# Optimization experiments

Hardware: AMD Instinct MI355X
Metric: run time of the kernel (lower is better)

The kernel has to match this reference:

```python
import jax, jax.numpy as jnp
import numpy as np

B, S, H = 2, 2048, 4096
NH, NKV, HD = 32, 8, 128
Q_SIZE, KV_SIZE = NH * HD, NKV * HD
ROPE_THETA = 10000.0


def setup_inputs() -> dict:
    key = jax.random.key(0)
    k1, k2, k3 = jax.random.split(key, 3)
    positions = jnp.tile(jnp.arange(S, dtype=jnp.int64 if jax.config.jax_enable_x64 else jnp.int32), (B, 1))
    hidden_states = jax.random.normal(k1, (B, S, H), dtype=jnp.float32)
    w_qkv = jax.random.normal(k2, (H, Q_SIZE + 2 * KV_SIZE), dtype=jnp.float32) * 0.02
    w_o = jax.random.normal(k3, (Q_SIZE, H), dtype=jnp.float32) * 0.02
    return {"positions": positions, "hidden_states": hidden_states, "w_qkv": w_qkv, "w_o": w_o}


def _apply_rope(x, positions):
    # x: [B, S, nheads, HD]; neox-style rotate-half RoPE
    half = HD // 2
    inv_freq = 1.0 / (ROPE_THETA ** (jnp.arange(0, half, dtype=jnp.float32) / half))
    freqs = positions.astype(jnp.float32)[..., None] * inv_freq  # [B, S, HD/2]
    cos = jnp.cos(freqs)[:, :, None, :]  # [B, S, 1, HD/2]
    sin = jnp.sin(freqs)[:, :, None, :]
    x1, x2 = x[..., :half], x[..., half:]
    return jnp.concatenate([x1 * cos - x2 * sin, x2 * cos + x1 * sin], axis=-1)


def reference(positions, hidden_states, w_qkv, w_o):
    qkv = jnp.einsum("bsh,hd->bsd", hidden_states, w_qkv)
    q = qkv[..., :Q_SIZE].reshape(B, S, NH, HD)
    k = qkv[..., Q_SIZE:Q_SIZE + KV_SIZE].reshape(B, S, NKV, HD)
    v = qkv[..., Q_SIZE + KV_SIZE:].reshape(B, S, NKV, HD)

    q = _apply_rope(q, positions)
    k = _apply_rope(k, positions)

    # GQA: expand kv heads to match query heads
    rep = NH // NKV
    k = jnp.repeat(k, rep, axis=2)  # [B, S, NH, HD]
    v = jnp.repeat(v, rep, axis=2)

    scale = 1.0 / jnp.sqrt(jnp.float32(HD))
    scores = jnp.einsum("bqhd,bkhd->bhqk", q, k) * scale  # [B, NH, S, S]
    causal = jnp.tril(jnp.ones((S, S), dtype=bool))
    scores = jnp.where(causal[None, None], scores, jnp.finfo(scores.dtype).min)
    probs = jax.nn.softmax(scores, axis=-1)

    attn = jnp.einsum("bhqk,bkhd->bqhd", probs, v).reshape(B, S, Q_SIZE)
    return jnp.einsum("bsd,dh->bsh", attn, w_o)
```

## Files before the change

### kernel.cpp

```cpp
#include <hip/hip_runtime.h>
#include <hip/hip_bf16.h>
#include <math.h>


typedef __attribute__((ext_vector_type(8))) __bf16 bf16x8;
typedef __attribute__((ext_vector_type(4))) float floatx4;

__device__ __forceinline__ floatx4 mfma16(bf16x8 a, bf16x8 b, floatx4 c) {
    return __builtin_amdgcn_mfma_f32_16x16x32_bf16(a, b, c, 0, 0, 0);
}

__device__ __forceinline__ void load_lds16(const __hip_bfloat16* g,
                                           __hip_bfloat16* lds_base_uniform) {
    __builtin_amdgcn_global_load_lds(
        (const __attribute__((address_space(1))) unsigned int*)g,
        (__attribute__((address_space(3))) unsigned int*)lds_base_uniform,
        16, 0, 0);
}

__global__ __launch_bounds__(256)
void convert_kernel(const float* __restrict__ in, __hip_bfloat16* __restrict__ out,
                    int n) {
    int i = (blockIdx.x * 256 + threadIdx.x) * 4;
    if (i >= n) return;
    float4 v = *(const float4*)(in + i);
    union { __hip_bfloat16 h[4]; uint2 u; } pk;
    pk.h[0] = __float2bfloat16(v.x);
    pk.h[1] = __float2bfloat16(v.y);
    pk.h[2] = __float2bfloat16(v.z);
    pk.h[3] = __float2bfloat16(v.w);
    *(uint2*)(out + i) = pk.u;
}

__global__ __launch_bounds__(256)
void transpose_f32_bf16_kernel(const float* __restrict__ in,
                               __hip_bfloat16* __restrict__ out, int R, int C) {
    __shared__ __hip_bfloat16 tile[64][65];
    const int r0 = blockIdx.y * 64, c0 = blockIdx.x * 64;
    const int t = threadIdx.x;
    #pragma unroll
    for (int i = 0; i < 16; ++i) {
        int idx = t + 256 * i;
        int rl = idx >> 6, cl = idx & 63;
        tile[rl][cl] = __float2bfloat16(in[(size_t)(r0 + rl) * C + (c0 + cl)]);
    }
    __syncthreads();
    #pragma unroll
    for (int i = 0; i < 16; ++i) {
        int idx = t + 256 * i;
        int cl = idx >> 6, rl = idx & 63;
        out[(size_t)(c0 + cl) * R + (r0 + rl)] = tile[rl][cl];
    }
}

__global__ __launch_bounds__(256)
void transpose_bf16_kernel(const __hip_bfloat16* __restrict__ in,
                           __hip_bfloat16* __restrict__ out, int R, int C) {
    __shared__ __hip_bfloat16 tile[64][65];
    const int bz = blockIdx.z;
    const __hip_bfloat16* inb  = in  + (size_t)bz * R * C;
    __hip_bfloat16*       outb = out + (size_t)bz * R * C;
    const int r0 = blockIdx.y * 64, c0 = blockIdx.x * 64;
    const int t = threadIdx.x;
    #pragma unroll
    for (int i = 0; i < 16; ++i) {
        int idx = t + 256 * i;
        int rl = idx >> 6, cl = idx & 63;
        tile[rl][cl] = inb[(size_t)(r0 + rl) * C + (c0 + cl)];
    }
    __syncthreads();
    #pragma unroll
    for (int i = 0; i < 16; ++i) {
        int idx = t + 256 * i;
        int cl = idx >> 6, rl = idx & 63;
        outb[(size_t)(c0 + cl) * R + (r0 + rl)] = tile[rl][cl];
    }
}

template <int MODE>
__global__ __launch_bounds__(256)
void gemm_bt_kernel(const __hip_bfloat16* __restrict__ A,
                    const __hip_bfloat16* __restrict__ Bt,
                    float* __restrict__ Cp,
                    __hip_bfloat16* __restrict__ Qr,
                    __hip_bfloat16* __restrict__ Kr,
                    __hip_bfloat16* __restrict__ Vv,
                    int M, int N, int K) {
    __shared__ __align__(16) __hip_bfloat16 As[128 * 32];
    __shared__ __align__(16) __hip_bfloat16 Bs[128 * 32];

    const int m0 = blockIdx.y * 128, n0 = blockIdx.x * 128;
    const int tid  = threadIdx.x;
    const int wave = tid >> 6, lane = tid & 63;
    const int quad = lane >> 4, l16 = lane & 15;
    const int wm = (wave >> 1) * 64, wn = (wave & 1) * 64;

    floatx4 acc[4][4] = {};

    for (int kt = 0; kt < K; kt += 32) {
        #pragma unroll
        for (int i = 0; i < 2; ++i) {
            int idx = tid + 256 * i;
            int row = idx >> 2;
            int kc  = (idx & 3) << 3;
            __hip_bfloat16* dstA = &As[(size_t)(wave * 64 + 256 * i) * 8];
            __hip_bfloat16* dstB = &Bs[(size_t)(wave * 64 + 256 * i) * 8];
            load_lds16(&A [(size_t)(m0 + row) * K + kt + kc], dstA);
            load_lds16(&Bt[(size_t)(n0 + row) * K + kt + kc], dstB);
        }
        __syncthreads();

        bf16x8 af[4], bfv[4];
        #pragma unroll
        for (int i = 0; i < 4; ++i)
            af[i]  = *(const bf16x8*)(&As[(wm + i * 16 + l16) * 32 + quad * 8]);
        #pragma unroll
        for (int j = 0; j < 4; ++j)
            bfv[j] = *(const bf16x8*)(&Bs[(wn + j * 16 + l16) * 32 + quad * 8]);
        #pragma unroll
        for (int i = 0; i < 4; ++i)
            #pragma unroll
            for (int j = 0; j < 4; ++j)
                acc[i][j] = mfma16(af[i], bfv[j], acc[i][j]);
        __syncthreads();
    }

    #pragma unroll
    for (int i = 0; i < 4; ++i) {
        #pragma unroll
        for (int j = 0; j < 4; ++j) {
            int col = n0 + wn + j * 16 + l16;
            #pragma unroll
            for (int r = 0; r < 4; ++r) {
                int row = m0 + wm + i * 16 + quad * 4 + r;
                if (MODE == 0) {
                    Cp[(size_t)row * N + col] = acc[i][j][r];
                } else {
                    __hip_bfloat16 v = __float2bfloat16(acc[i][j][r]);
                    int bb = row >> 11, s = row & 2047;
                    int d  = col & 127;
                    if (col < 4096) {
                        int h = col >> 7;
                        Qr[(((size_t)bb * 32 + h) * 2048 + s) * 128 + d] = v;
                    } else if (col < 5120) {
                        int kvh = (col - 4096) >> 7;
                        Kr[(((size_t)bb * 8 + kvh) * 2048 + s) * 128 + d] = v;
                    } else {
                        int kvh = (col - 5120) >> 7;
                        Vv[(((size_t)bb * 8 + kvh) * 2048 + s) * 128 + d] = v;
                    }
                }
            }
        }
    }
}

__global__ __launch_bounds__(256)
void rope_kernel(__hip_bfloat16* __restrict__ x,
                 const int* __restrict__ positions, int nrows, int bshift,
                 float qscale) {
    int gid = blockIdx.x * 256 + threadIdx.x;
    if (gid >= nrows * 64) return;
    int row = gid >> 6, d = gid & 63;
    int s = row & 2047;
    int b = row >> bshift;
    float p = (float)positions[(b << 11) + s];
    float ang = p * expf(-0.14391156831212787f * (float)d);
    float sn, cs;
    sincosf(ang, &sn, &cs);
    __hip_bfloat16* ptr = x + (size_t)row * 128;
    float x1 = __bfloat162float(ptr[d]);
    float x2 = __bfloat162float(ptr[d + 64]);
    ptr[d]      = __float2bfloat16((x1 * cs - x2 * sn) * qscale);
    ptr[d + 64] = __float2bfloat16((x2 * cs + x1 * sn) * qscale);
}

__device__ __forceinline__ void stage_tiles(const __hip_bfloat16* __restrict__ Kb,
                                            const __hip_bfloat16* __restrict__ Vb,
                                            int ks,
                                            __hip_bfloat16* KsBuf,
                                            __hip_bfloat16* VsBuf,
                                            int tid, int wave) {
    #pragma unroll
    for (int p = 0; p < 2; ++p) {
        int idx  = tid + 256 * p;
        int krow = idx >> 4, kc16 = idx & 15;
        load_lds16(&Kb[(size_t)(ks + krow) * 128 + ((kc16 ^ (krow & 7)) << 3)],
                   &KsBuf[(wave * 64 + 256 * p) * 8]);
        int vrow = idx >> 2, vc16 = idx & 3;
        load_lds16(&Vb[(size_t)vrow * 2048 + ks + ((vc16 ^ (vrow & 3)) << 3)],
                   &VsBuf[(wave * 64 + 256 * p) * 8]);
    }
}

__global__ __launch_bounds__(256)
void attn_kernel(const __hip_bfloat16* __restrict__ Qr,
                 const __hip_bfloat16* __restrict__ Kr,
                 const __hip_bfloat16* __restrict__ Vt,
                 __hip_bfloat16* __restrict__ Ao) {
    __shared__ __align__(16) __hip_bfloat16 Ks[2][32 * 128];
    __shared__ __align__(16) __hip_bfloat16 Vs[2][128 * 32];
    __shared__ __align__(16) __hip_bfloat16 Pl[4][32 * 32];

    const int tid  = threadIdx.x;
    const int wave = tid >> 6, lane = tid & 63;
    const int quad = lane >> 4, l16 = lane & 15;
    const int qb = (blockIdx.y & 16) ? blockIdx.x : (15 - blockIdx.x);
    const int q0 = qb * 128;
    const int qr0 = q0 + wave * 32;
    const int h  = blockIdx.y;
    const int b  = blockIdx.z;
    const int kv = h >> 2;

    const __hip_bfloat16* Qb = Qr + ((size_t)b * 32 + h)  * 2048 * 128;
    const __hip_bfloat16* Kb = Kr + ((size_t)b * 8  + kv) * 2048 * 128;
    const __hip_bfloat16* Vb = Vt + ((size_t)b * 8  + kv) * 128 * 2048;

    bf16x8 qf[2][4];
    #pragma unroll
    for (int i = 0; i < 2; ++i)
        #pragma unroll
        for (int kc = 0; kc < 4; ++kc)
            qf[i][kc] = *(const bf16x8*)(
                &Qb[(size_t)(qr0 + i * 16 + l16) * 128 + kc * 32 + quad * 8]);

    float m_i[2][4];
    #pragma unroll
    for (int i = 0; i < 2; ++i)
        #pragma unroll
        for (int r = 0; r < 4; ++r) m_i[i][r] = -1e30f;
    floatx4 o[2][8] = {};
    floatx4 lsum[2] = {};

    bf16x8 ones;
    #pragma unroll
    for (int e = 0; e < 8; ++e) ones[e] = (__bf16)1.0f;

    const int ntiles = (q0 >> 5) + 4;

    stage_tiles(Kb, Vb, 0, Ks[0], Vs[0], tid, wave);
    __syncthreads();

    int cur = 0;
    for (int t = 0; t < ntiles; ++t) {
        const int ks = t << 5;

        if (t + 1 < ntiles)
            stage_tiles(Kb, Vb, ks + 32, Ks[cur ^ 1], Vs[cur ^ 1], tid, wave);

        if (ks <= qr0 + 31) {
            const __hip_bfloat16* Kc = Ks[cur];
            const __hip_bfloat16* Vc = Vs[cur];
            const bool fullt = (ks + 31 <= qr0);

            floatx4 sacc[2][2] = {};
            __builtin_amdgcn_s_setprio(1);
            #pragma unroll
            for (int j = 0; j < 2; ++j) {
                #pragma unroll
                for (int kc = 0; kc < 4; ++kc) {
                    bf16x8 kf = *(const bf16x8*)(
                        &Kc[(j * 16 + l16) * 128 +
                            (((kc * 4 + quad) ^ (l16 & 7)) << 3)]);
                    #pragma unroll
                    for (int i = 0; i < 2; ++i)
                        sacc[i][j] = mfma16(qf[i][kc], kf, sacc[i][j]);
                }
            }
            __builtin_amdgcn_s_setprio(0);

            #pragma unroll
            for (int i = 0; i < 2; ++i) {
                #pragma unroll
                for (int r = 0; r < 4; ++r) {
                    int row = qr0 + i * 16 + quad * 4 + r;
                    float s0 = sacc[i][0][r];
                    float s1 = sacc[i][1][r];
                    if (!fullt) {
                        if (ks + l16 > row)      s0 = -1e30f;
                        if (ks + 16 + l16 > row) s1 = -1e30f;
                    }
                    float mx = fmaxf(s0, s1);
                    #pragma unroll
                    for (int off = 1; off < 16; off <<= 1)
                        mx = fmaxf(mx, __shfl_xor(mx, off, 64));
                    float mnew = fmaxf(m_i[i][r], mx);
                    float a  = __expf(m_i[i][r] - mnew);
                    float p0 = __expf(s0 - mnew);
                    float p1 = __expf(s1 - mnew);
                    int prow = i * 16 + quad * 4 + r;
                    Pl[wave][prow * 32 + (((l16 >> 3) ^ r) << 3) + (l16 & 7)] =
                        __float2bfloat16(p0);
                    Pl[wave][prow * 32 + (((2 + (l16 >> 3)) ^ r) << 3) + (l16 & 7)] =
                        __float2bfloat16(p1);
                    m_i[i][r] = mnew;
                    lsum[i][r] *= a;
                    #pragma unroll
                    for (int dn = 0; dn < 8; ++dn)
                        o[i][dn][r] *= a;
                }
            }

            bf16x8 pf[2];
            #pragma unroll
            for (int i = 0; i < 2; ++i)
                pf[i] = *(const bf16x8*)(
                    &Pl[wave][(i * 16 + l16) * 32 + ((quad ^ (l16 & 3)) << 3)]);

            __builtin_amdgcn_s_setprio(1);
            #pragma unroll
            for (int i = 0; i < 2; ++i)
                lsum[i] = mfma16(pf[i], ones, lsum[i]);
            #pragma unroll
            for (int dn = 0; dn < 8; ++dn) {
                bf16x8 vf = *(const bf16x8*)(
                    &Vc[(dn * 16 + l16) * 32 + ((quad ^ (l16 & 3)) << 3)]);
                #pragma unroll
                for (int i = 0; i < 2; ++i)
                    o[i][dn] = mfma16(pf[i], vf, o[i][dn]);
            }
            __builtin_amdgcn_s_setprio(0);
        }
        __syncthreads();
        cur ^= 1;
    }

    #pragma unroll
    for (int i = 0; i < 2; ++i) {
        #pragma unroll
        for (int r = 0; r < 4; ++r) {
            float inv = 1.0f / lsum[i][r];
            int row = qr0 + i * 16 + quad * 4 + r;
            size_t base = ((size_t)b * 2048 + row) * 4096 + (size_t)h * 128;
            #pragma unroll
            for (int dn = 0; dn < 8; ++dn)
                Ao[base + dn * 16 + l16] = __float2bfloat16(o[i][dn][r] * inv);
        }
    }
}

extern "C" void kernel_launch(void* const* d_in, const int* in_sizes, int n_in,
                              void* d_out, int out_size, void* d_ws, size_t ws_size,
                              hipStream_t stream) {
    const int*   positions = (const int*)d_in[0];
    const float* hidden    = (const float*)d_in[1];
    const float* wqkv      = (const float*)d_in[2];
    const float* wo        = (const float*)d_in[3];
    float* out = (float*)d_out;

    __hip_bfloat16* WqkvT = (__hip_bfloat16*)d_ws;
    __hip_bfloat16* WoT   = WqkvT + 25165824;
    __hip_bfloat16* Hb    = WoT   + 16777216;
    __hip_bfloat16* Qr    = Hb    + 16777216;
    __hip_bfloat16* Kr    = Qr    + 16777216;
    __hip_bfloat16* Vv    = Kr    + 4194304;
    __hip_bfloat16* Ao    = WqkvT;
    __hip_bfloat16* Vt    = Hb;

    convert_kernel<<<16777216 / 1024, 256, 0, stream>>>(hidden, Hb, 16777216);
    transpose_f32_bf16_kernel<<<dim3(6144 / 64, 4096 / 64), 256, 0, stream>>>(
        wqkv, WqkvT, 4096, 6144);
    transpose_f32_bf16_kernel<<<dim3(4096 / 64, 4096 / 64), 256, 0, stream>>>(
        wo, WoT, 4096, 4096);

    gemm_bt_kernel<1><<<dim3(6144 / 128, 4096 / 128), 256, 0, stream>>>(
        Hb, WqkvT, nullptr, Qr, Kr, Vv, 4096, 6144, 4096);

    rope_kernel<<<(131072 * 64) / 256, 256, 0, stream>>>(
        Qr, positions, 131072, 16, 0.08838834764831845f);
    rope_kernel<<<(32768  * 64) / 256, 256, 0, stream>>>(
        Kr, positions, 32768, 14, 1.0f);

    transpose_bf16_kernel<<<dim3(128 / 64, 2048 / 64, 16), 256, 0, stream>>>(
        Vv, Vt, 2048, 128);

    attn_kernel<<<dim3(2048 / 128, 32, 2), 256, 0, stream>>>(Qr, Kr, Vt, Ao);

    gemm_bt_kernel<0><<<dim3(4096 / 128, 4096 / 128), 256, 0, stream>>>(
        Ao, WoT, out, nullptr, nullptr, nullptr, 4096, 4096, 4096);
}
```

Before: 1.011 ms.

## Triple-buffer GEMM with async LDS loads, XOR swizzle, and larger tiles

```diff
diff --git a/kernel.cpp b/kernel.cpp
--- a/kernel.cpp
+++ b/kernel.cpp
@@ -16,6 +16,19 @@
         (const __attribute__((address_space(1))) unsigned int*)g,
         (__attribute__((address_space(3))) unsigned int*)lds_base_uniform,
         16, 0, 0);
+}
+
+__device__ __forceinline__ void sync_vm6() {
+    __builtin_amdgcn_sched_barrier(0);
+    asm volatile("s_waitcnt vmcnt(6)" ::: "memory");
+    __builtin_amdgcn_s_barrier();
+    __builtin_amdgcn_sched_barrier(0);
+}
+__device__ __forceinline__ void sync_vm0() {
+    __builtin_amdgcn_sched_barrier(0);
+    asm volatile("s_waitcnt vmcnt(0)" ::: "memory");
+    __builtin_amdgcn_s_barrier();
+    __builtin_amdgcn_sched_barrier(0);
 }
 
 __global__ __launch_bounds__(256)
@@ -78,7 +91,7 @@
 }
 
 template <int MODE>
-__global__ __launch_bounds__(256)
+__global__ __launch_bounds__(512)
 void gemm_bt_kernel(const __hip_bfloat16* __restrict__ A,
                     const __hip_bfloat16* __restrict__ Bt,
                     float* __restrict__ Cp,
@@ -86,43 +99,70 @@
                     __hip_bfloat16* __restrict__ Kr,
                     __hip_bfloat16* __restrict__ Vv,
                     int M, int N, int K) {
-    __shared__ __align__(16) __hip_bfloat16 As[128 * 32];
-    __shared__ __align__(16) __hip_bfloat16 Bs[128 * 32];
-
-    const int m0 = blockIdx.y * 128, n0 = blockIdx.x * 128;
+    __shared__ __align__(16) __hip_bfloat16 As[3][128 * 64];
+    __shared__ __align__(16) __hip_bfloat16 Bs[3][256 * 64];
+
+    const int m0 = blockIdx.y * 128, n0 = blockIdx.x * 256;
     const int tid  = threadIdx.x;
     const int wave = tid >> 6, lane = tid & 63;
     const int quad = lane >> 4, l16 = lane & 15;
-    const int wm = (wave >> 1) * 64, wn = (wave & 1) * 64;
+    const int wm = (wave >> 2) * 64, wn = (wave & 3) * 64;
+    const int srow = tid >> 3, sg = tid & 7;
 
     floatx4 acc[4][4] = {};
 
-    for (int kt = 0; kt < K; kt += 32) {
-        #pragma unroll
-        for (int i = 0; i < 2; ++i) {
-            int idx = tid + 256 * i;
-            int row = idx >> 2;
-            int kc  = (idx & 3) << 3;
-            __hip_bfloat16* dstA = &As[(size_t)(wave * 64 + 256 * i) * 8];
-            __hip_bfloat16* dstB = &Bs[(size_t)(wave * 64 + 256 * i) * 8];
-            load_lds16(&A [(size_t)(m0 + row) * K + kt + kc], dstA);
-            load_lds16(&Bt[(size_t)(n0 + row) * K + kt + kc], dstB);
-        }
-        __syncthreads();
-
-        bf16x8 af[4], bfv[4];
-        #pragma unroll
-        for (int i = 0; i < 4; ++i)
-            af[i]  = *(const bf16x8*)(&As[(wm + i * 16 + l16) * 32 + quad * 8]);
-        #pragma unroll
-        for (int j = 0; j < 4; ++j)
-            bfv[j] = *(const bf16x8*)(&Bs[(wn + j * 16 + l16) * 32 + quad * 8]);
-        #pragma unroll
-        for (int i = 0; i < 4; ++i)
-            #pragma unroll
-            for (int j = 0; j < 4; ++j)
-                acc[i][j] = mfma16(af[i], bfv[j], acc[i][j]);
-        __syncthreads();
+    auto stage = [&](int kt, int c) {
+        #pragma unroll
+        for (int r = 0; r < 2; ++r) {
+            int row = srow + 64 * r;
+            load_lds16(&A[(size_t)(m0 + row) * K + kt + ((sg ^ (row & 7)) << 3)],
+                       &As[c][(wave * 64 + 512 * r) * 8]);
+        }
+        #pragma unroll
+        for (int r = 0; r < 4; ++r) {
+            int row = srow + 64 * r;
+            load_lds16(&Bt[(size_t)(n0 + row) * K + kt + ((sg ^ (row & 7)) << 3)],
+                       &Bs[c][(wave * 64 + 512 * r) * 8]);
+        }
+    };
+
+    auto compute = [&](int c) {
+        #pragma unroll
+        for (int kk = 0; kk < 2; ++kk) {
+            bf16x8 af[4], bf[4];
+            #pragma unroll
+            for (int i = 0; i < 4; ++i) {
+                int row = wm + i * 16 + l16;
+                af[i] = *(const bf16x8*)(
+                    &As[c][row * 64 + (((kk * 4 + quad) ^ (row & 7)) << 3)]);
+            }
+            #pragma unroll
+            for (int j = 0; j < 4; ++j) {
+                int row = wn + j * 16 + l16;
+                bf[j] = *(const bf16x8*)(
+                    &Bs[c][row * 64 + (((kk * 4 + quad) ^ (row & 7)) << 3)]);
+            }
+            __builtin_amdgcn_s_setprio(1);
+            #pragma unroll
+            for (int i = 0; i < 4; ++i)
+                #pragma unroll
+                for (int j = 0; j < 4; ++j)
+                    acc[i][j] = mfma16(af[i], bf[j], acc[i][j]);
+            __builtin_amdgcn_s_setprio(0);
+        }
+    };
+
+    const int NT = K >> 6;
+    stage(0, 0);
+    stage(64, 1);
+    int cc = 0;
+    #pragma unroll 1
+    for (int t = 0; t < NT; ++t) {
+        if (t < NT - 1) sync_vm6(); else sync_vm0();
+        int cs = cc + 2; if (cs >= 3) cs -= 3;
+        if (t + 2 < NT) stage((t + 2) << 6, cs);
+        compute(cc);
+        if (++cc == 3) cc = 0;
     }
 
     #pragma unroll
@@ -363,7 +403,7 @@
     transpose_f32_bf16_kernel<<<dim3(4096 / 64, 4096 / 64), 256, 0, stream>>>(
         wo, WoT, 4096, 4096);
 
-    gemm_bt_kernel<1><<<dim3(6144 / 128, 4096 / 128), 256, 0, stream>>>(
+    gemm_bt_kernel<1><<<dim3(6144 / 256, 4096 / 128), 512, 0, stream>>>(
         Hb, WqkvT, nullptr, Qr, Kr, Vv, 4096, 6144, 4096);
 
     rope_kernel<<<(131072 * 64) / 256, 256, 0, stream>>>(
@@ -376,6 +416,6 @@
 
     attn_kernel<<<dim3(2048 / 128, 32, 2), 256, 0, stream>>>(Qr, Kr, Vt, Ao);
 
-    gemm_bt_kernel<0><<<dim3(4096 / 128, 4096 / 128), 256, 0, stream>>>(
+    gemm_bt_kernel<0><<<dim3(4096 / 256, 4096 / 128), 512, 0, stream>>>(
         Ao, WoT, out, nullptr, nullptr, nullptr, 4096, 4096, 4096);
 }
```

New measurement: 1.005 ms. About the same (-0.6%).
